# Optimization experiments

Hardware: AMD Instinct MI355X
Metric: run time of the kernel (lower is better)

The kernel has to match this reference:

```python
import jax, jax.numpy as jnp
import numpy as np

DIM = 2048

def setup_inputs() -> dict:
    key = jax.random.key(0)
    k_x, k_q, k_k, k_v, k_o = jax.random.split(key, 5)
    scale = 1.0 / np.sqrt(DIM)
    x = jax.random.normal(k_x, (2, 4096, DIM), dtype=jnp.float32)
    # nn.Linear weights are [out, in]; y = x @ W^T
    wq = jax.random.normal(k_q, (DIM, DIM), dtype=jnp.float32) * scale
    wk = jax.random.normal(k_k, (DIM, DIM), dtype=jnp.float32) * scale
    wv = jax.random.normal(k_v, (DIM, DIM), dtype=jnp.float32) * scale
    wo = jax.random.normal(k_o, (DIM, DIM), dtype=jnp.float32) * scale
    return {"x": x, "wq": wq, "wk": wk, "wv": wv, "wo": wo}

def reference(x, wq, wk, wv, wo):
    # Faithful to the torch module: NO head split; full-dim QK^T, scale by sqrt(dim).
    q = jnp.einsum('bsd,ed->bse', x, wq)
    k = jnp.einsum('bsd,ed->bse', x, wk)
    v = jnp.einsum('bsd,ed->bse', x, wv)
    scores = jnp.einsum('bqd,bkd->bqk', q, k) / jnp.sqrt(jnp.asarray(DIM, x.dtype))
    attn = jax.nn.softmax(scores, axis=-1)
    ctx = jnp.einsum('bqk,bkd->bqd', attn, v)
    return jnp.einsum('bsd,ed->bse', ctx, wo)
```

## Files before the change

### kernel.cpp

```cpp
#include <hip/hip_runtime.h>
#include <hip/hip_bf16.h>
#include <stdint.h>
#include <math.h>

typedef __attribute__((ext_vector_type(4))) float f32x4;
typedef __attribute__((ext_vector_type(8))) short s16x8;

typedef const __attribute__((address_space(1))) void* gas_ptr;
typedef __attribute__((address_space(3))) void* las_ptr;

__device__ __forceinline__ float bf2f(unsigned short u) {
    union { unsigned int i; float f; } x; x.i = ((unsigned int)u) << 16; return x.f;
}
__device__ __forceinline__ unsigned short f2bf(float f) {
    union { float f; unsigned int u; } x; x.f = f;
    unsigned int r = x.u + 0x7FFFu + ((x.u >> 16) & 1u);
    return (unsigned short)(r >> 16);
}

__global__ __launch_bounds__(256) void cvt_f32_bf16(const float* __restrict__ src,
                                                    unsigned short* __restrict__ dst,
                                                    long n) {
    long i = ((long)blockIdx.x * 256 + threadIdx.x) * 8;
    if (i + 8 > n) return;
    f32x4 a = *(const f32x4*)(src + i);
    f32x4 b = *(const f32x4*)(src + i + 4);
    s16x8 o;
    o[0] = (short)f2bf(a[0]); o[1] = (short)f2bf(a[1]);
    o[2] = (short)f2bf(a[2]); o[3] = (short)f2bf(a[3]);
    o[4] = (short)f2bf(b[0]); o[5] = (short)f2bf(b[1]);
    o[6] = (short)f2bf(b[2]); o[7] = (short)f2bf(b[3]);
    *(s16x8*)(dst + i) = o;
}

template <typename CT>
__global__ __launch_bounds__(512, 2)
void gemm256_bt(const unsigned short* __restrict__ A,
                const unsigned short* __restrict__ B,
                CT* __restrict__ C,
                int N, int K, int nt,
                long sA, long sB, long sC, float alpha)
{
    A += (long)blockIdx.z * sA;
    B += (long)blockIdx.z * sB;
    C += (long)blockIdx.z * sC;

    __shared__ unsigned short L[2][2][2][128][64];

    const int t    = threadIdx.x;
    const int lane = t & 63;
    const int wid  = t >> 6;
    const int wm   = wid >> 2;
    const int wn   = wid & 3;

    const int cpx = (int)gridDim.x >> 3;
    const int bx  = ((int)blockIdx.x & 7) * cpx + ((int)blockIdx.x >> 3);
    const long brow = (long)bx * 256;
    const long bcol = (long)blockIdx.y * 256;

    const int lr = lane & 15;
    const int hi = lane >> 4;
    const int sw = (lr & 7) << 3;

    int voff[2];
    const unsigned short* pA[2][2];
    const unsigned short* pB[2][2];
    {
        const unsigned short* Ab = A + brow * K;
        const unsigned short* Bb = B + bcol * K;
        #pragma unroll
        for (int j = 0; j < 2; ++j) {
            int u  = t + 512 * j;
            int ix = u >> 3;
            int cg = u & 7;
            int cs = (cg * 8) ^ ((ix & 7) << 3);
            voff[j] = u * 8;
            long ra0 = ((long)(ix >> 6) << 7) | (0 << 6) | (ix & 63);
            long ra1 = ((long)(ix >> 6) << 7) | (1 << 6) | (ix & 63);
            long rb0 = ((long)(ix >> 5) << 6) | (0 << 5) | (ix & 31);
            long rb1 = ((long)(ix >> 5) << 6) | (1 << 5) | (ix & 31);
            pA[0][j] = Ab + ra0 * K + cs;
            pA[1][j] = Ab + ra1 * K + cs;
            pB[0][j] = Bb + rb0 * K + cs;
            pB[1][j] = Bb + rb1 * K + cs;
        }
    }

#define STAGE_A(H, KT) do { \
    _Pragma("unroll") \
    for (int j = 0; j < 2; ++j) \
        __builtin_amdgcn_global_load_lds((gas_ptr)(pA[H][j] + (long)(KT) * 64), \
            (las_ptr)(&L[(KT) & 1][0][H][0][0] + voff[j]), 16, 0, 0); \
} while (0)
#define STAGE_B(H, KT) do { \
    _Pragma("unroll") \
    for (int j = 0; j < 2; ++j) \
        __builtin_amdgcn_global_load_lds((gas_ptr)(pB[H][j] + (long)(KT) * 64), \
            (las_ptr)(&L[(KT) & 1][1][H][0][0] + voff[j]), 16, 0, 0); \
} while (0)

#define LOAD_AF(DST, CUR, QM) do { \
    _Pragma("unroll") \
    for (int m = 0; m < 4; ++m) \
        _Pragma("unroll") \
        for (int kk = 0; kk < 2; ++kk) \
            DST[m][kk] = *(const s16x8*)&L[CUR][0][QM][wm * 64 + m * 16 + lr][(kk * 32 + hi * 8) ^ sw]; \
} while (0)
#define LOAD_BQ(DST, CUR, QN) do { \
    _Pragma("unroll") \
    for (int n = 0; n < 2; ++n) \
        _Pragma("unroll") \
        for (int kk = 0; kk < 2; ++kk) \
            DST[n][kk] = *(const s16x8*)&L[CUR][1][QN][wn * 32 + n * 16 + lr][(kk * 32 + hi * 8) ^ sw]; \
} while (0)
#define MFMA_Q(QM, QN, AF, BQ) do { \
    _Pragma("unroll") \
    for (int m = 0; m < 4; ++m) \
        _Pragma("unroll") \
        for (int n = 0; n < 2; ++n) \
            _Pragma("unroll") \
            for (int kk = 0; kk < 2; ++kk) \
                acc[(QM) * 4 + m][(QN) * 2 + n] = __builtin_amdgcn_mfma_f32_16x16x32_bf16( \
                    AF[m][kk], BQ[n][kk], acc[(QM) * 4 + m][(QN) * 2 + n], 0, 0, 0); \
} while (0)

#define TILE_BODY(CUR, KTE, BQ0) do { \
    const int kt_ = (KTE); \
     \
    LOAD_AF(af0, CUR, 0); \
    LOAD_BQ(BQ0, CUR, 0); \
    LOAD_BQ(bq1, CUR, 1); \
    if (kt_ + 1 < nt) { \
        STAGE_A(0, kt_ + 1); STAGE_B(0, kt_ + 1); \
        STAGE_A(1, kt_ + 1); STAGE_B(1, kt_ + 1); \
    } \
    __builtin_amdgcn_s_setprio(1); \
    MFMA_Q(0, 0, af0, BQ0); \
    MFMA_Q(0, 1, af0, bq1); \
    __builtin_amdgcn_s_setprio(0); \
     \
    LOAD_AF(af1, CUR, 1); \
    __builtin_amdgcn_s_setprio(1); \
    MFMA_Q(1, 1, af1, bq1); \
    MFMA_Q(1, 0, af1, BQ0); \
    __builtin_amdgcn_s_setprio(0); \
     \
    if (kt_ + 1 < nt) { \
        asm volatile("s_waitcnt vmcnt(0)" ::: "memory"); \
        __builtin_amdgcn_s_barrier(); \
        asm volatile("" ::: "memory"); \
    } \
} while (0)

    f32x4 acc[8][4];
    #pragma unroll
    for (int m = 0; m < 8; ++m)
        #pragma unroll
        for (int n = 0; n < 4; ++n)
            acc[m][n] = {0.f, 0.f, 0.f, 0.f};

    s16x8 af0[4][2], af1[4][2], bq0E[2][2], bq0O[2][2], bq1[2][2];

    STAGE_A(0, 0); STAGE_B(0, 0); STAGE_A(1, 0); STAGE_B(1, 0);
    asm volatile("s_waitcnt vmcnt(0)" ::: "memory");
    __builtin_amdgcn_s_barrier();
    asm volatile("" ::: "memory");

    for (int kt = 0; kt < nt; kt += 2) {
        TILE_BODY(0, kt, bq0E);
        if (kt + 1 < nt) TILE_BODY(1, kt + 1, bq0O);
    }
#undef TILE_BODY
#undef STAGE_A
#undef STAGE_B
#undef LOAD_AF
#undef LOAD_BQ
#undef MFMA_Q

    #pragma unroll
    for (int m = 0; m < 8; ++m) {
        #pragma unroll
        for (int n = 0; n < 4; ++n) {
            #pragma unroll
            for (int i = 0; i < 4; ++i) {
                long row = brow + wm * 128 + m * 16 + hi * 4 + i;
                long col = bcol + wn * 64 + n * 16 + lr;
                float vv = acc[m][n][i] * alpha;
                if constexpr (sizeof(CT) == 2) {
                    ((unsigned short*)C)[row * (long)N + col] = f2bf(vv);
                } else {
                    ((float*)C)[row * (long)N + col] = vv;
                }
            }
        }
    }
}

__global__ __launch_bounds__(256) void transpose_bf16(const unsigned short* __restrict__ src,
                                                      unsigned short* __restrict__ dst,
                                                      int srows, int scols) {
    __shared__ unsigned short tile[64][66];
    const long bofs = (long)blockIdx.z * srows * scols;
    const unsigned short* s = src + bofs;
    unsigned short* d = dst + bofs;
    const int c0 = blockIdx.x * 64;
    const int r0 = blockIdx.y * 64;
    const int tx = threadIdx.x & 15;
    const int ty = threadIdx.x >> 4;

    #pragma unroll
    for (int k = 0; k < 4; ++k) {
        int r = ty + 16 * k;
        ushort4 v = *(const ushort4*)(s + (long)(r0 + r) * scols + c0 + tx * 4);
        tile[r][tx * 4 + 0] = v.x; tile[r][tx * 4 + 1] = v.y;
        tile[r][tx * 4 + 2] = v.z; tile[r][tx * 4 + 3] = v.w;
    }
    __syncthreads();
    #pragma unroll
    for (int k = 0; k < 4; ++k) {
        int dr = ty + 16 * k;
        ushort4 v;
        v.x = tile[tx * 4 + 0][dr]; v.y = tile[tx * 4 + 1][dr];
        v.z = tile[tx * 4 + 2][dr]; v.w = tile[tx * 4 + 3][dr];
        *(ushort4*)(d + (long)(c0 + dr) * srows + r0 + tx * 4) = v;
    }
}

__global__ __launch_bounds__(256) void softmax_inplace(unsigned short* __restrict__ S, int ncols) {
    const long row = blockIdx.x;
    unsigned short* p = S + row * (long)ncols;
    const int t = threadIdx.x;
    const int wid = t >> 6;

    ushort4 raw[4];
    const ushort4* pv = (const ushort4*)(p + t * 16);
    #pragma unroll
    for (int i = 0; i < 4; ++i) raw[i] = pv[i];

    float v[16];
    float mx = -1e30f;
    #pragma unroll
    for (int i = 0; i < 4; ++i) {
        v[4*i+0] = bf2f(raw[i].x); v[4*i+1] = bf2f(raw[i].y);
        v[4*i+2] = bf2f(raw[i].z); v[4*i+3] = bf2f(raw[i].w);
    }
    #pragma unroll
    for (int i = 0; i < 16; ++i) mx = fmaxf(mx, v[i]);
    #pragma unroll
    for (int off = 32; off > 0; off >>= 1) mx = fmaxf(mx, __shfl_xor(mx, off));

    __shared__ float red[8];
    if ((t & 63) == 0) red[wid] = mx;
    __syncthreads();
    mx = fmaxf(fmaxf(red[0], red[1]), fmaxf(red[2], red[3]));

    float sum = 0.f;
    #pragma unroll
    for (int i = 0; i < 16; ++i) { v[i] = __expf(v[i] - mx); sum += v[i]; }
    #pragma unroll
    for (int off = 32; off > 0; off >>= 1) sum += __shfl_xor(sum, off);
    __syncthreads();
    if ((t & 63) == 0) red[4 + wid] = sum;
    __syncthreads();
    sum = red[4] + red[5] + red[6] + red[7];
    const float inv = 1.0f / sum;

    ushort4* po = (ushort4*)(p + t * 16);
    #pragma unroll
    for (int i = 0; i < 4; ++i) {
        ushort4 o;
        o.x = f2bf(v[4*i+0] * inv); o.y = f2bf(v[4*i+1] * inv);
        o.z = f2bf(v[4*i+2] * inv); o.w = f2bf(v[4*i+3] * inv);
        po[i] = o;
    }
}

extern "C" void kernel_launch(void* const* d_in, const int* in_sizes, int n_in,
                              void* d_out, int out_size, void* d_ws, size_t ws_size,
                              hipStream_t stream) {
    const float* x  = (const float*)d_in[0];
    const float* wq = (const float*)d_in[1];
    const float* wk = (const float*)d_in[2];
    const float* wv = (const float*)d_in[3];
    const float* wo = (const float*)d_in[4];
    float* out = (float*)d_out;

    const long SDIM = 2048, SEQ = 4096, BATCH = 2;
    const long MS = BATCH * SEQ;
    const long XN = MS * SDIM;
    const long WN = SDIM * SDIM;

    unsigned short* ws  = (unsigned short*)d_ws;
    unsigned short* Xbf = ws;
    unsigned short* Wqb = ws + XN;
    unsigned short* Wkb = Wqb + WN;
    unsigned short* Wvb = Wkb + WN;
    unsigned short* Wob = Wvb + WN;
    unsigned short* Qb  = Wob + WN;
    unsigned short* Kb  = Qb + XN;
    unsigned short* Vb  = Kb + XN;
    unsigned short* Sb  = Vb + XN;
    unsigned short* Vt  = Xbf;
    unsigned short* Ctx = Qb;

    cvt_f32_bf16<<<(int)(XN / 2048), 256, 0, stream>>>(x,  Xbf, XN);
    cvt_f32_bf16<<<(int)(WN / 2048), 256, 0, stream>>>(wq, Wqb, WN);
    cvt_f32_bf16<<<(int)(WN / 2048), 256, 0, stream>>>(wk, Wkb, WN);
    cvt_f32_bf16<<<(int)(WN / 2048), 256, 0, stream>>>(wv, Wvb, WN);
    cvt_f32_bf16<<<(int)(WN / 2048), 256, 0, stream>>>(wo, Wob, WN);

    dim3 gp((unsigned)(MS / 256), (unsigned)(SDIM / 256), 1);
    gemm256_bt<unsigned short><<<gp, 512, 0, stream>>>(Xbf, Wqb, Qb, (int)SDIM, (int)SDIM, (int)(SDIM / 64), 0, 0, 0, 1.0f);
    gemm256_bt<unsigned short><<<gp, 512, 0, stream>>>(Xbf, Wkb, Kb, (int)SDIM, (int)SDIM, (int)(SDIM / 64), 0, 0, 0, 1.0f);
    gemm256_bt<unsigned short><<<gp, 512, 0, stream>>>(Xbf, Wvb, Vb, (int)SDIM, (int)SDIM, (int)(SDIM / 64), 0, 0, 0, 1.0f);

    dim3 gt((unsigned)(SDIM / 64), (unsigned)(SEQ / 64), (unsigned)BATCH);
    transpose_bf16<<<gt, 256, 0, stream>>>(Vb, Vt, (int)SEQ, (int)SDIM);

    const float scale = 1.0f / sqrtf((float)SDIM);
    dim3 gs((unsigned)(SEQ / 256), (unsigned)(SEQ / 256), (unsigned)BATCH);
    gemm256_bt<unsigned short><<<gs, 512, 0, stream>>>(Qb, Kb, Sb, (int)SEQ, (int)SDIM, (int)(SDIM / 64),
                                                       SEQ * SDIM, SEQ * SDIM, SEQ * SEQ, scale);

    softmax_inplace<<<(int)(BATCH * SEQ), 256, 0, stream>>>(Sb, (int)SEQ);

    dim3 gc((unsigned)(SEQ / 256), (unsigned)(SDIM / 256), (unsigned)BATCH);
    gemm256_bt<unsigned short><<<gc, 512, 0, stream>>>(Sb, Vt, Ctx, (int)SDIM, (int)SEQ, (int)(SEQ / 64),
                                                       SEQ * SEQ, SDIM * SEQ, SEQ * SDIM, 1.0f);

    gemm256_bt<float><<<gp, 512, 0, stream>>>(Ctx, Wob, out, (int)SDIM, (int)SDIM, (int)(SDIM / 64), 0, 0, 0, 1.0f);
}
```

Before: 550.5 us.

## Software-pipeline GEMM main loop so second-half MFMAs overlap next tile's loads

Restructures the GEMM k-loop into a rotated software pipeline. The second half of each tile's MFMAs (af1 quadrants) now runs after the barrier, in the next iteration, before the LDS fragment loads for the next tile. The af1 fragment is loaded before the barrier, so the LDS buffer can be overwritten afterwards. The aim is to hide barrier and LDS latency behind MFMA work, at the cost of a prologue/epilogue and an extra lgkmcnt wait.

```diff
diff --git a/kernel.cpp b/kernel.cpp
--- a/kernel.cpp
+++ b/kernel.cpp
@@ -124,34 +124,6 @@
                     AF[m][kk], BQ[n][kk], acc[(QM) * 4 + m][(QN) * 2 + n], 0, 0, 0); \
 } while (0)
 
-#define TILE_BODY(CUR, KTE, BQ0) do { \
-    const int kt_ = (KTE); \
-     \
-    LOAD_AF(af0, CUR, 0); \
-    LOAD_BQ(BQ0, CUR, 0); \
-    LOAD_BQ(bq1, CUR, 1); \
-    if (kt_ + 1 < nt) { \
-        STAGE_A(0, kt_ + 1); STAGE_B(0, kt_ + 1); \
-        STAGE_A(1, kt_ + 1); STAGE_B(1, kt_ + 1); \
-    } \
-    __builtin_amdgcn_s_setprio(1); \
-    MFMA_Q(0, 0, af0, BQ0); \
-    MFMA_Q(0, 1, af0, bq1); \
-    __builtin_amdgcn_s_setprio(0); \
-     \
-    LOAD_AF(af1, CUR, 1); \
-    __builtin_amdgcn_s_setprio(1); \
-    MFMA_Q(1, 1, af1, bq1); \
-    MFMA_Q(1, 0, af1, BQ0); \
-    __builtin_amdgcn_s_setprio(0); \
-     \
-    if (kt_ + 1 < nt) { \
-        asm volatile("s_waitcnt vmcnt(0)" ::: "memory"); \
-        __builtin_amdgcn_s_barrier(); \
-        asm volatile("" ::: "memory"); \
-    } \
-} while (0)
-
     f32x4 acc[8][4];
     #pragma unroll
     for (int m = 0; m < 8; ++m)
@@ -159,18 +131,55 @@
         for (int n = 0; n < 4; ++n)
             acc[m][n] = {0.f, 0.f, 0.f, 0.f};
 
-    s16x8 af0[4][2], af1[4][2], bq0E[2][2], bq0O[2][2], bq1[2][2];
+    s16x8 af0[4][2], af1[4][2], bq0[2][2], bq1[2][2];
 
     STAGE_A(0, 0); STAGE_B(0, 0); STAGE_A(1, 0); STAGE_B(1, 0);
     asm volatile("s_waitcnt vmcnt(0)" ::: "memory");
     __builtin_amdgcn_s_barrier();
     asm volatile("" ::: "memory");
 
-    for (int kt = 0; kt < nt; kt += 2) {
-        TILE_BODY(0, kt, bq0E);
-        if (kt + 1 < nt) TILE_BODY(1, kt + 1, bq0O);
-    }
-#undef TILE_BODY
+    LOAD_AF(af0, 0, 0);
+    LOAD_BQ(bq0, 0, 0);
+    LOAD_BQ(bq1, 0, 1);
+    if (nt > 1) {
+        STAGE_A(0, 1); STAGE_B(0, 1);
+        STAGE_A(1, 1); STAGE_B(1, 1);
+    }
+    __builtin_amdgcn_s_setprio(1);
+    MFMA_Q(0, 0, af0, bq0);
+    MFMA_Q(0, 1, af0, bq1);
+    __builtin_amdgcn_s_setprio(0);
+    LOAD_AF(af1, 0, 1);
+    asm volatile("s_waitcnt lgkmcnt(0)" ::: "memory");
+    asm volatile("s_waitcnt vmcnt(0)" ::: "memory");
+    __builtin_amdgcn_s_barrier();
+    asm volatile("" ::: "memory");
+
+    for (int kt = 1; kt < nt; ++kt) {
+        const int cur = kt & 1;
+        __builtin_amdgcn_s_setprio(1);
+        MFMA_Q(1, 1, af1, bq1);
+        MFMA_Q(1, 0, af1, bq0);
+        __builtin_amdgcn_s_setprio(0);
+        LOAD_AF(af0, cur, 0);
+        LOAD_BQ(bq0, cur, 0);
+        LOAD_BQ(bq1, cur, 1);
+        if (kt + 1 < nt) {
+            STAGE_A(0, kt + 1); STAGE_B(0, kt + 1);
+            STAGE_A(1, kt + 1); STAGE_B(1, kt + 1);
+        }
+        __builtin_amdgcn_s_setprio(1);
+        MFMA_Q(0, 0, af0, bq0);
+        MFMA_Q(0, 1, af0, bq1);
+        __builtin_amdgcn_s_setprio(0);
+        LOAD_AF(af1, cur, 1);
+        asm volatile("s_waitcnt lgkmcnt(0)" ::: "memory");
+        asm volatile("s_waitcnt vmcnt(0)" ::: "memory");
+        __builtin_amdgcn_s_barrier();
+        asm volatile("" ::: "memory");
+    }
+    MFMA_Q(1, 1, af1, bq1);
+    MFMA_Q(1, 0, af1, bq0);
 #undef STAGE_A
 #undef STAGE_B
 #undef LOAD_AF
```

Measured after the change: 538.1 us. -2.2%, faster.
